# Optimization experiments

Hardware: AMD Instinct MI355X
Metric: run time of the kernel (lower is better)

## Reference

```python
import jax, jax.numpy as jnp
import numpy as np

_LEVELS = jnp.array([-4, -2, -1, 0, 1, 2, 4], dtype=jnp.int32)  # shift-quant 7-value grid 'A'

B, S = 1, 512
IN_F, OUT_F = 4096, 16384
BLOCK = 64
NUM_BLOCKS = (IN_F + BLOCK - 1) // BLOCK  # 64


def setup_inputs() -> dict:
    key = jax.random.key(0)
    k1, k2, k3, k4 = jax.random.split(key, 4)
    x = jax.random.normal(k1, (B, S, IN_F), dtype=jnp.float32)
    idx = jax.random.randint(k2, (OUT_F, IN_F), 0, 7)
    q_weight = _LEVELS[idx]  # int32 values in {-4,-2,-1,0,1,2,4}
    scales = (jax.random.uniform(k3, (OUT_F, NUM_BLOCKS), dtype=jnp.float32) * 0.05 + 0.001).astype(jnp.float16)
    bias = (jax.random.normal(k4, (OUT_F,), dtype=jnp.float32) * 0.02).astype(jnp.float16)
    return {"x": x, "q_weight": q_weight, "scales": scales, "bias": bias, "block_size": BLOCK}


def reference(x, q_weight, scales, bias, block_size):
    # shift_matmul: dequantize blockwise-scaled power-of-two int8 weights, then GEMM.
    out_f, in_f = q_weight.shape
    # broadcast per-block fp16 scales along the in_features axis (handles padding block)
    w_scale = jnp.repeat(scales.astype(jnp.float32), block_size, axis=1)[:, :in_f]  # [out, in]
    w = q_weight.astype(jnp.float32) * w_scale  # [out, in]
    out = jnp.einsum("bsi,oi->bso", x, w)
    out = out + bias.astype(out.dtype)
    return out.astype(x.dtype)
```

## Files before the change

### kernel.cpp

```cpp
#include <hip/hip_runtime.h>
#include <hip/hip_bf16.h>
#include <stdint.h>


#define MM 512
#define NN 16384
#define KK 4096
#define BN 64
#define BK 128
#define NKB (KK / BK)
#define NSLAB (NN / BN)

typedef __bf16 bf16x8 __attribute__((ext_vector_type(8)));
typedef float floatx4 __attribute__((ext_vector_type(4)));

__device__ __forceinline__ unsigned int pk_bf16_rtn(float lo, float hi) {
    __hip_bfloat162 h = __float22bfloat162_rn(float2{lo, hi});
    return *reinterpret_cast<unsigned int*>(&h);
}

__device__ __forceinline__ void gload16(const void* g, void* l) {
    __builtin_amdgcn_global_load_lds(
        (const __attribute__((address_space(1))) void*)g,
        (__attribute__((address_space(3))) void*)l, 16, 0, 0);
}

__global__ __launch_bounds__(256) void pack_x(const float* __restrict__ x,
                                              unsigned short* __restrict__ xp) {
    const int t    = blockIdx.x * 256 + threadIdx.x;
    const int lane = t & 63;
    const int mt   = (t >> 6) & 31;
    const int ks   = (t >> 11) & 3;
    const int kb   = t >> 13;
    const int m    = mt * 16 + (lane & 15);
    const int k    = kb * 128 + ks * 32 + (lane >> 4) * 8;
    const float* px = x + (size_t)m * KK + k;
    const float4 a = *(const float4*)px;
    const float4 b = *(const float4*)(px + 4);
    uint4 o;
    o.x = pk_bf16_rtn(a.x, a.y);
    o.y = pk_bf16_rtn(a.z, a.w);
    o.z = pk_bf16_rtn(b.x, b.y);
    o.w = pk_bf16_rtn(b.z, b.w);
    *(uint4*)(xp + (size_t)t * 8) = o;
}

__global__ __launch_bounds__(256) void pack_w(const int* __restrict__ qw,
                                              const float* __restrict__ scales,
                                              unsigned short* __restrict__ wb) {
    __shared__ unsigned short lw[64][132];
    __shared__ float ls[128];
    const int tile = blockIdx.x;
    const int slab = tile >> 5;
    const int kb   = tile & 31;
    const int u    = threadIdx.x;

    if (u < 128)
        ls[u] = scales[(size_t)(slab * 64 + (u >> 1)) * 64 + kb * 2 + (u & 1)];
    __syncthreads();

    const int* qbase = qw + (size_t)slab * 64 * KK + kb * 128;
#pragma unroll
    for (int i = 0; i < 8; ++i) {
        const int c  = i * 256 + u;
        const int r  = c >> 5;
        const int kk = (c & 31) * 4;
        const int4 q = *(const int4*)(qbase + (size_t)r * KK + kk);
        const float s = ls[r * 2 + ((c & 31) >> 4)];
        uint2 o;
        o.x = pk_bf16_rtn((float)q.x * s, (float)q.y * s);
        o.y = pk_bf16_rtn((float)q.z * s, (float)q.w * s);
        *(uint2*)&lw[r][kk] = o;
    }
    __syncthreads();

    unsigned short* wt = wb + (size_t)tile * 8192;
#pragma unroll
    for (int hc = 0; hc < 4; ++hc) {
        const int c  = hc * 256 + u;
        const int f  = c >> 6;
        const int l  = c & 63;
        const int ks = f >> 2;
        const int j  = f & 3;
        const uint4 v = *(const uint4*)&lw[j * 16 + (l & 15)][ks * 32 + (l >> 4) * 8];
        *(uint4*)(wt + (size_t)c * 8) = v;
    }
}

#define STAGE_B(KB, BUF)                                                        \
    {                                                                           \
        const unsigned short* src_ = wbase + (size_t)(KB) * 8192 + (size_t)t * 8; \
        gload16(src_,           &sB[BUF][wv * 512]);                            \
        gload16(src_ + 512 * 8, &sB[BUF][4096 + wv * 512]);                     \
    }

#define LOAD_A(DST, KB)                                                         \
    {                                                                           \
        const unsigned short* ap_ =                                             \
            xp + (size_t)(KB) * 65536                                           \
               + (size_t)((h * 16 + wv * 2) * 64 + lane) * 8;                   \
        _Pragma("unroll")                                                       \
        for (int ks = 0; ks < 4; ++ks) {                                        \
            DST[ks][0] = *(const bf16x8*)(ap_ + ks * 16384);                    \
            DST[ks][1] = *(const bf16x8*)(ap_ + ks * 16384 + 512);              \
        }                                                                       \
    }

#define COMPUTE(BUF, A)                                                         \
    {                                                                           \
        const unsigned short* sb_ = sB[BUF];                                    \
        _Pragma("unroll")                                                       \
        for (int ks = 0; ks < 4; ++ks) {                                        \
            _Pragma("unroll")                                                   \
            for (int jj = 0; jj < 4; jj += 2) {                                 \
                bf16x8 b0 = *(const bf16x8*)(sb_ + ((ks * 4 + jj) * 64 + lane) * 8);     \
                bf16x8 b1 = *(const bf16x8*)(sb_ + ((ks * 4 + jj + 1) * 64 + lane) * 8); \
                acc[0][jj]     = __builtin_amdgcn_mfma_f32_16x16x32_bf16(A[ks][0], b0, acc[0][jj], 0, 0, 0);     \
                acc[1][jj]     = __builtin_amdgcn_mfma_f32_16x16x32_bf16(A[ks][1], b0, acc[1][jj], 0, 0, 0);     \
                acc[0][jj + 1] = __builtin_amdgcn_mfma_f32_16x16x32_bf16(A[ks][0], b1, acc[0][jj + 1], 0, 0, 0); \
                acc[1][jj + 1] = __builtin_amdgcn_mfma_f32_16x16x32_bf16(A[ks][1], b1, acc[1][jj + 1], 0, 0, 0); \
            }                                                                   \
        }                                                                       \
    }

__global__ __launch_bounds__(512, 4) void qlin_gemm(
    const unsigned short* __restrict__ xp,
    const unsigned short* __restrict__ wb,
    const float* __restrict__ bias,
    float* __restrict__ out)
{
    __shared__ unsigned short sB[2][BN * BK];

    const int t    = threadIdx.x;
    const int lane = t & 63;
    const int wv   = t >> 6;
    const int ln   = lane & 15;
    const int quad = lane >> 4;
    const int slab = blockIdx.x & 255;
    const int h    = blockIdx.x >> 8;
    const int n0   = slab * BN;

    const unsigned short* wbase = wb + (size_t)slab * 32 * 8192;

    floatx4 acc[2][4];
#pragma unroll
    for (int i = 0; i < 2; ++i)
#pragma unroll
        for (int j = 0; j < 4; ++j)
            acc[i][j] = (floatx4)0.0f;

    bf16x8 aA[4][2], aB[4][2];

    STAGE_B(0, 0)
    LOAD_A(aA, 0)
    __syncthreads();

    for (int kb = 0; kb < NKB; kb += 2) {
        STAGE_B(kb + 1, 1)
        LOAD_A(aB, kb + 1)
        COMPUTE(0, aA)
        __syncthreads();

        if (kb + 2 < NKB) {
            STAGE_B(kb + 2, 0)
            LOAD_A(aA, kb + 2)
        }
        COMPUTE(1, aB)
        if (kb + 2 < NKB) __syncthreads();
    }

#pragma unroll
    for (int j = 0; j < 4; ++j) {
        const int n = n0 + j * 16 + ln;
        const float bv = bias[n];
#pragma unroll
        for (int i = 0; i < 2; ++i) {
            const int mbase = h * 256 + wv * 32 + i * 16 + quad * 4;
#pragma unroll
            for (int rr = 0; rr < 4; ++rr)
                out[(size_t)(mbase + rr) * NN + n] = acc[i][j][rr] + bv;
        }
    }
}

__global__ __launch_bounds__(256) void qlin_naive(
    const float* __restrict__ x, const int* __restrict__ qw,
    const float* __restrict__ scales, const float* __restrict__ bias,
    float* __restrict__ out) {
    const int n = blockIdx.x * 256 + threadIdx.x;
    const int m = blockIdx.y;
    if (n >= NN || m >= MM) return;
    float accv = 0.0f;
    for (int kb = 0; kb < 64; ++kb) {
        const float s = scales[(size_t)n * 64 + kb];
        float part = 0.0f;
        for (int k = kb * 64; k < kb * 64 + 64; ++k)
            part += x[(size_t)m * KK + k] * (float)qw[(size_t)n * KK + k];
        accv += part * s;
    }
    out[(size_t)m * NN + n] = accv + bias[n];
}

extern "C" void kernel_launch(void* const* d_in, const int* in_sizes, int n_in,
                              void* d_out, int out_size, void* d_ws, size_t ws_size,
                              hipStream_t stream) {
    const float* x    = (const float*)d_in[0];
    const int* qw     = (const int*)d_in[1];
    const float* scl  = (const float*)d_in[2];
    const float* bias = (const float*)d_in[3];
    float* out        = (float*)d_out;

    const size_t XPB = (size_t)MM * KK * sizeof(unsigned short);
    const size_t WBB = (size_t)NN * KK * sizeof(unsigned short);

    if (ws_size >= XPB + WBB) {
        unsigned short* xp = (unsigned short*)d_ws;
        unsigned short* wb = (unsigned short*)((char*)d_ws + XPB);
        pack_x<<<dim3(MM * KK / (256 * 8)), dim3(256), 0, stream>>>(x, xp);
        pack_w<<<dim3(NSLAB * 32), dim3(256), 0, stream>>>(qw, scl, wb);
        qlin_gemm<<<dim3(NSLAB * 2), dim3(512), 0, stream>>>(xp, wb, bias, out);
    } else {
        qlin_naive<<<dim3(NN / 256, MM), dim3(256), 0, stream>>>(x, qw, scl, bias, out);
    }
}
```

Before: 493.2 us.

## Fuse weight dequantization into GEMM with producer-consumer warp specialization

Removes the separate weight pre-pack kernel and its bf16 workspace. Dedicated producer wavefronts inside the GEMM block load int32 weights, apply per-block scales, and write bf16 tiles into double-buffered LDS while consumer wavefronts run MFMA. Barriers wait only on LDS counters instead of draining all memory. This cuts the round-trip of the dequantized weight matrix through global memory, but each int32 weight slab is now read by both M-halves, and producer register and bandwidth pressure may limit the pipeline.

```diff
diff --git a/kernel.cpp b/kernel.cpp
--- a/kernel.cpp
+++ b/kernel.cpp
@@ -10,19 +10,20 @@
 #define BK 128
 #define NKB (KK / BK)
 #define NSLAB (NN / BN)
+#define NCTHR 512
+#define NPTHR 128
+#define NTHR (NCTHR + NPTHR)
 
 typedef __bf16 bf16x8 __attribute__((ext_vector_type(8)));
 typedef float floatx4 __attribute__((ext_vector_type(4)));
+
+__device__ __forceinline__ void barrier_nodrain() {
+    asm volatile("s_waitcnt lgkmcnt(0)\n\ts_barrier" ::: "memory");
+}
 
 __device__ __forceinline__ unsigned int pk_bf16_rtn(float lo, float hi) {
     __hip_bfloat162 h = __float22bfloat162_rn(float2{lo, hi});
     return *reinterpret_cast<unsigned int*>(&h);
-}
-
-__device__ __forceinline__ void gload16(const void* g, void* l) {
-    __builtin_amdgcn_global_load_lds(
-        (const __attribute__((address_space(1))) void*)g,
-        (__attribute__((address_space(3))) void*)l, 16, 0, 0);
 }
 
 __global__ __launch_bounds__(256) void pack_x(const float* __restrict__ x,
@@ -45,55 +46,6 @@
     *(uint4*)(xp + (size_t)t * 8) = o;
 }
 
-__global__ __launch_bounds__(256) void pack_w(const int* __restrict__ qw,
-                                              const float* __restrict__ scales,
-                                              unsigned short* __restrict__ wb) {
-    __shared__ unsigned short lw[64][132];
-    __shared__ float ls[128];
-    const int tile = blockIdx.x;
-    const int slab = tile >> 5;
-    const int kb   = tile & 31;
-    const int u    = threadIdx.x;
-
-    if (u < 128)
-        ls[u] = scales[(size_t)(slab * 64 + (u >> 1)) * 64 + kb * 2 + (u & 1)];
-    __syncthreads();
-
-    const int* qbase = qw + (size_t)slab * 64 * KK + kb * 128;
-#pragma unroll
-    for (int i = 0; i < 8; ++i) {
-        const int c  = i * 256 + u;
-        const int r  = c >> 5;
-        const int kk = (c & 31) * 4;
-        const int4 q = *(const int4*)(qbase + (size_t)r * KK + kk);
-        const float s = ls[r * 2 + ((c & 31) >> 4)];
-        uint2 o;
-        o.x = pk_bf16_rtn((float)q.x * s, (float)q.y * s);
-        o.y = pk_bf16_rtn((float)q.z * s, (float)q.w * s);
-        *(uint2*)&lw[r][kk] = o;
-    }
-    __syncthreads();
-
-    unsigned short* wt = wb + (size_t)tile * 8192;
-#pragma unroll
-    for (int hc = 0; hc < 4; ++hc) {
-        const int c  = hc * 256 + u;
-        const int f  = c >> 6;
-        const int l  = c & 63;
-        const int ks = f >> 2;
-        const int j  = f & 3;
-        const uint4 v = *(const uint4*)&lw[j * 16 + (l & 15)][ks * 32 + (l >> 4) * 8];
-        *(uint4*)(wt + (size_t)c * 8) = v;
-    }
-}
-
-#define STAGE_B(KB, BUF)                                                        \
-    {                                                                           \
-        const unsigned short* src_ = wbase + (size_t)(KB) * 8192 + (size_t)t * 8; \
-        gload16(src_,           &sB[BUF][wv * 512]);                            \
-        gload16(src_ + 512 * 8, &sB[BUF][4096 + wv * 512]);                     \
-    }
-
 #define LOAD_A(DST, KB)                                                         \
     {                                                                           \
         const unsigned short* ap_ =                                             \
@@ -123,62 +75,117 @@
         }                                                                       \
     }
 
-__global__ __launch_bounds__(512, 4) void qlin_gemm(
+#define LOADQ(KB)                                                               \
+    {                                                                           \
+        _Pragma("unroll")                                                       \
+        for (int i = 0; i < 16; ++i) {                                          \
+            const int r_ = i * 4 + rb;                                          \
+            q[i] = *(const int4*)(qbase + (size_t)r_ * KK + (size_t)(KB) * BK); \
+        }                                                                       \
+    }
+
+#define PRODUCE(KB, BUF)                                                        \
+    {                                                                           \
+        unsigned short* sw_ = sB[BUF];                                          \
+        _Pragma("unroll")                                                       \
+        for (int i = 0; i < 16; ++i) {                                          \
+            const int r_   = i * 4 + rb;                                        \
+            const int sidx = ((ks4 + (r_ >> 4)) * 64 + (qo16 | (r_ & 15))) * 8 + e0; \
+            const float s_ = ls[r_][(KB) * 2 + bo];                             \
+            uint2 o_;                                                           \
+            o_.x = pk_bf16_rtn((float)q[i].x * s_, (float)q[i].y * s_);         \
+            o_.y = pk_bf16_rtn((float)q[i].z * s_, (float)q[i].w * s_);         \
+            *(uint2*)&sw_[sidx] = o_;                                           \
+        }                                                                       \
+    }
+
+__global__ __launch_bounds__(NTHR) void qlin_fused(
     const unsigned short* __restrict__ xp,
-    const unsigned short* __restrict__ wb,
+    const int* __restrict__ qw,
+    const float* __restrict__ scales,
     const float* __restrict__ bias,
     float* __restrict__ out)
 {
     __shared__ unsigned short sB[2][BN * BK];
+    __shared__ float ls[64][64];
 
     const int t    = threadIdx.x;
+    const int slab = blockIdx.x & 255;
+    const int h    = blockIdx.x >> 8;
+    const int n0   = slab * BN;
+
+    for (int i = t; i < 4096; i += NTHR)
+        ls[i >> 6][i & 63] = scales[(size_t)(n0 + (i >> 6)) * 64 + (i & 63)];
+
     const int lane = t & 63;
     const int wv   = t >> 6;
     const int ln   = lane & 15;
     const int quad = lane >> 4;
-    const int slab = blockIdx.x & 255;
-    const int h    = blockIdx.x >> 8;
-    const int n0   = slab * BN;
-
-    const unsigned short* wbase = wb + (size_t)slab * 32 * 8192;
-
     floatx4 acc[2][4];
-#pragma unroll
-    for (int i = 0; i < 2; ++i)
-#pragma unroll
-        for (int j = 0; j < 4; ++j)
-            acc[i][j] = (floatx4)0.0f;
-
     bf16x8 aA[4][2], aB[4][2];
 
-    STAGE_B(0, 0)
-    LOAD_A(aA, 0)
-    __syncthreads();
+    const int u    = t - NCTHR;
+    const int kk   = (u & 31) * 4;
+    const int rb   = u >> 5;
+    const int ks4  = (kk >> 5) * 4;
+    const int qo16 = ((kk >> 3) & 3) << 4;
+    const int e0   = kk & 7;
+    const int bo   = kk >> 6;
+    const int* qbase = qw + (size_t)n0 * KK + kk;
+    int4 q[16];
+
+    if (t >= NCTHR) {
+        LOADQ(0)
+    } else {
+#pragma unroll
+        for (int i = 0; i < 2; ++i)
+#pragma unroll
+            for (int j = 0; j < 4; ++j)
+                acc[i][j] = (floatx4)0.0f;
+        LOAD_A(aA, 0)
+    }
+    barrier_nodrain();
+
+    if (t >= NCTHR) {
+        PRODUCE(0, 0)
+        LOADQ(1)
+    }
+    barrier_nodrain();
 
     for (int kb = 0; kb < NKB; kb += 2) {
-        STAGE_B(kb + 1, 1)
-        LOAD_A(aB, kb + 1)
-        COMPUTE(0, aA)
-        __syncthreads();
-
-        if (kb + 2 < NKB) {
-            STAGE_B(kb + 2, 0)
-            LOAD_A(aA, kb + 2)
+        if (t < NCTHR) {
+            LOAD_A(aB, kb + 1)
+            COMPUTE(0, aA)
+        } else {
+            PRODUCE(kb + 1, 1)
+            if (kb + 2 < NKB) LOADQ(kb + 2)
         }
-        COMPUTE(1, aB)
-        if (kb + 2 < NKB) __syncthreads();
-    }
-
-#pragma unroll
-    for (int j = 0; j < 4; ++j) {
-        const int n = n0 + j * 16 + ln;
-        const float bv = bias[n];
-#pragma unroll
-        for (int i = 0; i < 2; ++i) {
-            const int mbase = h * 256 + wv * 32 + i * 16 + quad * 4;
-#pragma unroll
-            for (int rr = 0; rr < 4; ++rr)
-                out[(size_t)(mbase + rr) * NN + n] = acc[i][j][rr] + bv;
+        barrier_nodrain();
+
+        if (t < NCTHR) {
+            if (kb + 2 < NKB) LOAD_A(aA, kb + 2)
+            COMPUTE(1, aB)
+        } else {
+            if (kb + 2 < NKB) {
+                PRODUCE(kb + 2, 0)
+                if (kb + 3 < NKB) LOADQ(kb + 3)
+            }
+        }
+        if (kb + 2 < NKB) barrier_nodrain();
+    }
+
+    if (t < NCTHR) {
+#pragma unroll
+        for (int j = 0; j < 4; ++j) {
+            const int n = n0 + j * 16 + ln;
+            const float bv = bias[n];
+#pragma unroll
+            for (int i = 0; i < 2; ++i) {
+                const int mbase = h * 256 + wv * 32 + i * 16 + quad * 4;
+#pragma unroll
+                for (int rr = 0; rr < 4; ++rr)
+                    out[(size_t)(mbase + rr) * NN + n] = acc[i][j][rr] + bv;
+            }
         }
     }
 }
@@ -211,14 +218,11 @@
     float* out        = (float*)d_out;
 
     const size_t XPB = (size_t)MM * KK * sizeof(unsigned short);
-    const size_t WBB = (size_t)NN * KK * sizeof(unsigned short);
-
-    if (ws_size >= XPB + WBB) {
+
+    if (ws_size >= XPB) {
         unsigned short* xp = (unsigned short*)d_ws;
-        unsigned short* wb = (unsigned short*)((char*)d_ws + XPB);
         pack_x<<<dim3(MM * KK / (256 * 8)), dim3(256), 0, stream>>>(x, xp);
-        pack_w<<<dim3(NSLAB * 32), dim3(256), 0, stream>>>(qw, scl, wb);
-        qlin_gemm<<<dim3(NSLAB * 2), dim3(512), 0, stream>>>(xp, wb, bias, out);
+        qlin_fused<<<dim3(NSLAB * 2), dim3(NTHR), 0, stream>>>(xp, qw, scl, bias, out);
     } else {
         qlin_naive<<<dim3(NN / 256, MM), dim3(256), 0, stream>>>(x, qw, scl, bias, out);
     }
```

Result: slower. 896.9 us (+81.8%).
